# Optimization experiments

Hardware: AMD Instinct MI355X
Metric: run time of the kernel (lower is better)

## Reference

```python
import jax, jax.numpy as jnp
import numpy as np

B, T, D, NH, DK = 2, 2048, 1024, 16, 64
EPS = 1e-6

def proj_H(z):
    return z - z.mean(axis=-1, keepdims=True)

def to_clr(p):
    return proj_H(jnp.log(p + EPS))

def setup_inputs() -> dict:
    key = jax.random.key(0)
    ks = jax.random.split(key, 9)
    p = jax.random.uniform(ks[0], (B, T, D), dtype=jnp.float32)
    # xavier_uniform with gain=0.8 for square-ish [in,out] matrices
    def xavier(k, fan_in, fan_out):
        bound = 0.8 * np.sqrt(6.0 / (fan_in + fan_out))
        return jax.random.uniform(k, (fan_in, fan_out), minval=-bound, maxval=bound, dtype=jnp.float32)
    H = NH * DK
    Wq = xavier(ks[1], D, H); bq = jnp.zeros((H,), jnp.float32)
    Wk = xavier(ks[2], D, H); bk = jnp.zeros((H,), jnp.float32)
    Wv = xavier(ks[3], D, H); bv = jnp.zeros((H,), jnp.float32)
    Wo = xavier(ks[4], H, D); bo = jnp.zeros((D,), jnp.float32)
    return {"p": p, "Wq": Wq, "bq": bq, "Wk": Wk, "bk": bk,
            "Wv": Wv, "bv": bv, "Wo": Wo, "bo": bo}

def reference(p, Wq, bq, Wk, bk, Wv, bv, Wo, bo):
    z = to_clr(p)                                   # [B,T,D]
    # projections with H-projection epilogue, reshaped to [B,T,NH,DK]
    q = proj_H(z @ Wq + bq).reshape(B, T, NH, DK)
    k = proj_H(z @ Wk + bk).reshape(B, T, NH, DK)
    v = proj_H(z @ Wv + bv).reshape(B, T, NH, DK)
    att = jnp.einsum('bihd,bjhd->bhij', q, k) / jnp.sqrt(jnp.float32(DK))
    w = jax.nn.softmax(att, axis=-1)                # dropout is identity in eval
    z_out = jnp.einsum('bhij,bjhd->bihd', w, v).reshape(B, T, NH * DK)
    z_out = proj_H(z_out @ Wo + bo)
    return jax.nn.softmax(z_out, axis=-1)           # from_clr
```

## Files before the change

kernel.cpp:

```cpp
#include <hip/hip_runtime.h>

typedef unsigned short u16;
typedef __attribute__((ext_vector_type(8))) short short8_t;
typedef __attribute__((ext_vector_type(8))) _Float16 half8_t;
typedef __attribute__((ext_vector_type(4))) float f32x4;
typedef __attribute__((ext_vector_type(16))) float f32x16;
typedef __attribute__((ext_vector_type(4))) int int4v;

#define BB    2
#define TT    2048
#define DD    1024
#define NHEAD 16
#define DKH   64
#define HH    1024
#define MR    4096
#define CLR_EPS 1e-6f
#define QSCALE_CONST 0.18033688011112042f

#define O_WQKVT  0ull
#define O_WOT    6291456ull
#define O_WMEAN  8388608ull
#define O_BQKV   8404992ull
#define O_BO     8417280ull
#define O_Z      8421376ull
#define O_QKV    16809984ull
#define O_VT     41975808ull
#define O_ZOUT   50364416ull
#define O_LOGITS O_QKV

__device__ __forceinline__ u16 f2h(float f) {
  _Float16 h = (_Float16)f;
  return __builtin_bit_cast(u16, h);
}
__device__ __forceinline__ float h2f(u16 x) {
  return (float)__builtin_bit_cast(_Float16, x);
}

__device__ __forceinline__ f32x4 mfma16(short8_t a, short8_t b, f32x4 c) {
  return __builtin_amdgcn_mfma_f32_16x16x32_f16(
      __builtin_bit_cast(half8_t, a), __builtin_bit_cast(half8_t, b), c, 0, 0, 0);
}
__device__ __forceinline__ f32x16 mfma32(short8_t a, short8_t b, f32x16 c) {
  return __builtin_amdgcn_mfma_f32_32x32x16_f16(
      __builtin_bit_cast(half8_t, a), __builtin_bit_cast(half8_t, b), c, 0, 0, 0);
}

typedef const __attribute__((address_space(1))) unsigned int as1_u32_t;
typedef __attribute__((address_space(3))) unsigned int as3_u32_t;

__device__ __forceinline__ void async16(const void* g, void* l) {
  __builtin_amdgcn_global_load_lds((as1_u32_t*)g, (as3_u32_t*)l, 16, 0, 0);
}

__device__ __forceinline__ short8_t ldfrag(const u16* buf, int row, int kh, int lane) {
  const int byte = (row * 128 + ((kh * 32 + ((lane >> 4) << 3)) << 1)) ^ ((row & 7) << 4);
  return *(const short8_t*)((const char*)buf + byte);
}

__global__ __launch_bounds__(256) void wprep_mean(
    const float* __restrict__ Wq, const float* __restrict__ Wk,
    const float* __restrict__ Wv, const float* __restrict__ Wo,
    const float* __restrict__ bq, const float* __restrict__ bk,
    const float* __restrict__ bv, const float* __restrict__ bo,
    float* __restrict__ wmean, float* __restrict__ bqkv_p, float* __restrict__ bo_p) {
  __shared__ float sb[4];
  const int bid = blockIdx.x, tid = threadIdx.x;
  if (bid < 4096) {
    const int m = bid >> 10, d = bid & 1023;
    const float* Wm = (m == 0) ? Wq : (m == 1) ? Wk : (m == 2) ? Wv : Wo;
    float4 x = ((const float4*)(Wm + (size_t)d * 1024))[tid];
    float s = x.x + x.y + x.z + x.w;
    #pragma unroll
    for (int dd = 32; dd; dd >>= 1) s += __shfl_xor(s, dd);
    if ((tid & 63) == 0) sb[tid >> 6] = s;
    __syncthreads();
    if (tid == 0) wmean[bid] = (sb[0] + sb[1] + sb[2] + sb[3]) * (1.f / 1024.f);
  } else {
    const int j = bid - 4096;
    const float* bb = (j == 0) ? bq : (j == 1) ? bk : (j == 2) ? bv : bo;
    float4 x = ((const float4*)bb)[tid];
    float s = x.x + x.y + x.z + x.w;
    #pragma unroll
    for (int dd = 32; dd; dd >>= 1) s += __shfl_xor(s, dd);
    if ((tid & 63) == 0) sb[tid >> 6] = s;
    __syncthreads();
    const float mean = (sb[0] + sb[1] + sb[2] + sb[3]) * (1.f / 1024.f);
    float* dst = (j < 3) ? (bqkv_p + j * 1024) : bo_p;
    float4 o = {x.x - mean, x.y - mean, x.z - mean, x.w - mean};
    ((float4*)dst)[tid] = o;
  }
}

__global__ __launch_bounds__(256) void wprep_trans(
    const float* __restrict__ Wq, const float* __restrict__ Wk,
    const float* __restrict__ Wv, const float* __restrict__ Wo,
    const float* __restrict__ wmean, u16* __restrict__ wqkvt, u16* __restrict__ wot) {
  __shared__ float tl[64][65];
  const int tj = blockIdx.x, ti = blockIdx.y, m = blockIdx.z;
  const int tid = threadIdx.x;
  const float* Wm = (m == 0) ? Wq : (m == 1) ? Wk : (m == 2) ? Wv : Wo;
  const int d0 = ti * 64, h0 = tj * 64;
  #pragma unroll
  for (int rr = 0; rr < 4; ++rr) {
    const int r = (tid >> 4) + rr * 16;
    float4 x = *(const float4*)(Wm + (size_t)(d0 + r) * 1024 + h0 + ((tid & 15) << 2));
    const float mu = wmean[m * 1024 + d0 + r];
    tl[r][(tid & 15) * 4 + 0] = x.x - mu;
    tl[r][(tid & 15) * 4 + 1] = x.y - mu;
    tl[r][(tid & 15) * 4 + 2] = x.z - mu;
    tl[r][(tid & 15) * 4 + 3] = x.w - mu;
  }
  __syncthreads();
  #pragma unroll
  for (int rr = 0; rr < 2; ++rr) {
    const int hh = (tid >> 3) + rr * 32;
    const int cd = (tid & 7) << 3;
    short8_t v;
    #pragma unroll
    for (int i = 0; i < 8; ++i) v[i] = (short)f2h(tl[cd + i][hh]);
    u16* dst = (m < 3) ? (wqkvt + ((size_t)(m * 1024 + h0 + hh)) * 1024 + d0 + cd)
                       : (wot + ((size_t)(h0 + hh)) * 1024 + d0 + cd);
    *(short8_t*)dst = v;
  }
}

__global__ __launch_bounds__(256) void clr_kernel(const float* __restrict__ p, u16* __restrict__ z) {
  __shared__ float sb[4];
  const int r = blockIdx.x, tid = threadIdx.x;
  float4 x = ((const float4*)(p + (size_t)r * 1024))[tid];
  float l0 = __logf(x.x + CLR_EPS), l1 = __logf(x.y + CLR_EPS);
  float l2 = __logf(x.z + CLR_EPS), l3 = __logf(x.w + CLR_EPS);
  float s = l0 + l1 + l2 + l3;
  #pragma unroll
  for (int dd = 32; dd; dd >>= 1) s += __shfl_xor(s, dd);
  if ((tid & 63) == 0) sb[tid >> 6] = s;
  __syncthreads();
  const float mu = (sb[0] + sb[1] + sb[2] + sb[3]) * (1.f / 1024.f);
  ushort4 o;
  o.x = f2h(l0 - mu); o.y = f2h(l1 - mu); o.z = f2h(l2 - mu); o.w = f2h(l3 - mu);
  ((ushort4*)(z + (size_t)r * 1024))[tid] = o;
}

__global__ __launch_bounds__(256, 2) void gemm_qkv_8ph(
    const u16* __restrict__ A, const u16* __restrict__ Bt, const float* __restrict__ bias,
    u16* __restrict__ qkv, u16* __restrict__ vt) {
  __shared__ u16 As[2][128 * 64];
  __shared__ u16 Bs[2][192 * 64];
  const int tid = threadIdx.x, lane = tid & 63, w = tid >> 6;
  const int wm = w >> 1, wn = w & 1;
  const int id = blockIdx.x;
  const int x = id & 7, idx = id >> 3;
  const int mt = (x & 3) * 8 + (idx & 7);
  const int nt = (x >> 2) * 8 + (idx >> 3);
  const int m0 = mt * 128, n0 = nt * 192;
  const int srow = tid >> 3, schk = tid & 7;
  const int l15 = lane & 15, lg4 = (lane >> 4) << 2;

  f32x4 acc[4][6] = {};

  auto stA = [&](int k0, int buf) {
    #pragma unroll
    for (int u = 0; u < 4; ++u) {
      const int r = srow + u * 32;
      const int c = k0 + ((schk ^ (r & 7)) << 3);
      async16(A + (size_t)(m0 + r) * 1024 + c, &As[buf][r * 64 + schk * 8]);
    }
  };
  auto stB = [&](int k0, int buf) {
    #pragma unroll
    for (int u = 0; u < 6; ++u) {
      const int r = srow + u * 32;
      const int c = k0 + ((schk ^ (r & 7)) << 3);
      async16(Bt + (size_t)(n0 + r) * 1024 + c, &Bs[buf][r * 64 + schk * 8]);
    }
  };

  stA(0, 0); stB(0, 0);
  asm volatile("s_waitcnt vmcnt(0)" ::: "memory");
  __builtin_amdgcn_s_barrier();

  short8_t afr[4], bfr[6];
  for (int t = 0; t < 16; ++t) {
    const int cur = t & 1;
    const int k0n = ((t + 1) & 15) * 64;
    const u16* Ab = &As[cur][0];
    const u16* Bb_ = &Bs[cur][0];

    #pragma unroll
    for (int j = 0; j < 6; ++j) bfr[j] = ldfrag(Bb_, wn * 96 + j * 16 + l15, 0, lane);
    #pragma unroll
    for (int i = 0; i < 4; ++i) afr[i] = ldfrag(Ab, wm * 64 + i * 16 + l15, 0, lane);
    stA(k0n, cur ^ 1); stB(k0n, cur ^ 1);
    __builtin_amdgcn_s_barrier();
    asm volatile("s_waitcnt lgkmcnt(0)" ::: "memory");
    __builtin_amdgcn_sched_barrier(0);
    __builtin_amdgcn_s_setprio(1);
    #pragma unroll
    for (int i = 0; i < 4; ++i)
      #pragma unroll
      for (int j = 0; j < 6; ++j)
        acc[i][j] = mfma16(afr[i], bfr[j], acc[i][j]);
    __builtin_amdgcn_s_setprio(0);
    __builtin_amdgcn_s_barrier();

    #pragma unroll
    for (int j = 0; j < 6; ++j) bfr[j] = ldfrag(Bb_, wn * 96 + j * 16 + l15, 1, lane);
    #pragma unroll
    for (int i = 0; i < 4; ++i) afr[i] = ldfrag(Ab, wm * 64 + i * 16 + l15, 1, lane);
    __builtin_amdgcn_s_barrier();
    asm volatile("s_waitcnt lgkmcnt(0)" ::: "memory");
    __builtin_amdgcn_sched_barrier(0);
    __builtin_amdgcn_s_setprio(1);
    #pragma unroll
    for (int i = 0; i < 4; ++i)
      #pragma unroll
      for (int j = 0; j < 6; ++j)
        acc[i][j] = mfma16(afr[i], bfr[j], acc[i][j]);
    __builtin_amdgcn_s_setprio(0);
    asm volatile("s_waitcnt vmcnt(0)" ::: "memory");
    __builtin_amdgcn_s_barrier();
  }

  #pragma unroll
  for (int j = 0; j < 6; ++j) {
    const int col = n0 + wn * 96 + j * 16 + l15;
    const float bb = bias[col];
    if (col < 2048) {
      const float sc = (col < 1024) ? QSCALE_CONST : 1.0f;
      #pragma unroll
      for (int i = 0; i < 4; ++i) {
        const int rowb = m0 + wm * 64 + i * 16 + lg4;
        #pragma unroll
        for (int r = 0; r < 4; ++r)
          qkv[(size_t)(rowb + r) * 3072 + col] = f2h((acc[i][j][r] + bb) * sc);
      }
    } else {
      const int h = (col - 2048) >> 6, dk = col & 63;
      #pragma unroll
      for (int i = 0; i < 4; ++i) {
        const int rowb = m0 + wm * 64 + i * 16 + lg4;
        const int b = rowb >> 11, tq = rowb & 2047;
        const int k5 = tq & 31;
        const int pos = (tq & ~31) + (k5 & 16) + ((k5 & 4) << 1) + ((k5 & 8) >> 1);
        ushort4 pk;
        pk.x = f2h(acc[i][j][0] + bb);
        pk.y = f2h(acc[i][j][1] + bb);
        pk.z = f2h(acc[i][j][2] + bb);
        pk.w = f2h(acc[i][j][3] + bb);
        *(ushort4*)(vt + ((size_t)((b * NHEAD + h) * 64 + dk)) * TT + pos) = pk;
      }
    }
  }
}

__global__ __launch_bounds__(256) void gemm_bt(
    const u16* __restrict__ A, const u16* __restrict__ Bt, const float* __restrict__ bias,
    float* __restrict__ Cout, int Ndim, int Kdim) {
  __shared__ u16 As[2][128 * 64];
  __shared__ u16 Bs[2][128 * 64];
  const int tid = threadIdx.x;
  const int lane = tid & 63, wid = tid >> 6;
  const int m0 = blockIdx.y * 128, n0 = blockIdx.x * 128;
  const int wm = wid >> 1, wn = wid & 1;
  const int srow = tid >> 3, schk = tid & 7;
  f32x4 acc[4][4] = {};

  auto STG = [&](int k0, int buf) {
    #pragma unroll
    for (int rr = 0; rr < 4; ++rr) {
      const int row = srow + rr * 32;
      const int gcol = k0 + ((schk ^ (row & 7)) << 3);
      async16(A + (size_t)(m0 + row) * Kdim + gcol, &As[buf][row * 64 + schk * 8]);
      async16(Bt + (size_t)(n0 + row) * Kdim + gcol, &Bs[buf][row * 64 + schk * 8]);
    }
  };

  STG(0, 0);
  asm volatile("s_waitcnt vmcnt(0)" ::: "memory");
  __builtin_amdgcn_s_barrier();

  const int nt = Kdim >> 6;
  for (int t = 0; t < nt; ++t) {
    const int cur = t & 1;
    STG((((t + 1) & (nt - 1))) << 6, cur ^ 1);
    #pragma unroll
    for (int kk = 0; kk < 2; ++kk) {
      short8_t af[4], bf[4];
      #pragma unroll
      for (int i = 0; i < 4; ++i) {
        af[i] = ldfrag(&As[cur][0], wm * 64 + i * 16 + (lane & 15), kk, lane);
        bf[i] = ldfrag(&Bs[cur][0], wn * 64 + i * 16 + (lane & 15), kk, lane);
      }
      #pragma unroll
      for (int i = 0; i < 4; ++i)
        #pragma unroll
        for (int j = 0; j < 4; ++j)
          acc[i][j] = mfma16(af[i], bf[j], acc[i][j]);
    }
    asm volatile("s_waitcnt vmcnt(0)" ::: "memory");
    __builtin_amdgcn_s_barrier();
  }

  #pragma unroll
  for (int j = 0; j < 4; ++j) {
    const int col = n0 + wn * 64 + j * 16 + (lane & 15);
    const float bb = bias[col];
    #pragma unroll
    for (int i = 0; i < 4; ++i) {
      const int rowb = m0 + wm * 64 + i * 16 + ((lane >> 4) << 2);
      #pragma unroll
      for (int r = 0; r < 4; ++r)
        Cout[(size_t)(rowb + r) * Ndim + col] = acc[i][j][r] + bb;
    }
  }
}

__global__ __launch_bounds__(512, 2) void attn_kernel(
    const u16* __restrict__ qkv, const u16* __restrict__ vt, u16* __restrict__ zout) {
  __shared__ char smem[65536];
  const int id = blockIdx.x;
  const int qb = (id >> 3) & 7;
  const int bh = (id & 7) * 4 + (id >> 6);
  const int b = bh >> 4, h = bh & 15;
  const int tid = threadIdx.x, lane = tid & 63, w = tid >> 6;
  const int qw = w & 3, ks = w >> 2;
  const int hl = lane >> 5, l31 = lane & 31;
  const int swz = (l31 & 7) << 4;
  const int q0 = qb * 256 + qw * 64;

  short8_t qf[2][4];
  #pragma unroll
  for (int qt = 0; qt < 2; ++qt)
    #pragma unroll
    for (int c = 0; c < 4; ++c)
      qf[qt][c] = *(const short8_t*)(qkv + (size_t)(b * TT + q0 + qt * 32 + l31) * 3072
                                     + h * 64 + c * 16 + hl * 8);

  const int sr0 = qw * 16 + (lane >> 3);
  const int schk = lane & 7;
  const int scol = (schk ^ (sr0 & 7)) << 3;
  const int dof = sr0 * 128 + schk * 16;
  char* kls = smem + ks * 16384;
  char* vls = smem + 32768 + ks * 16384;
  const u16* kg = qkv + 1024 + (size_t)h * 64;
  const u16* vg = vt + ((size_t)(b * NHEAD + h) * 64 + sr0) * (size_t)TT;

  {
    const int kbase = ks * 1024;
    async16(kg + (size_t)(b * TT + kbase + sr0) * 3072 + scol, kls + dof);
    async16(kg + (size_t)(b * TT + kbase + sr0 + 8) * 3072 + scol, kls + dof + 1024);
    async16(vg + kbase + scol, vls + dof);
    async16(vg + (size_t)8 * TT + kbase + scol, vls + dof + 1024);
  }

  f32x16 o[2][2] = {};
  f32x16 lb[2] = {};
  short8_t ones;
  #pragma unroll
  for (int i = 0; i < 8; ++i) ones[i] = (short)0x3C00;

  for (int it = 0; it < 16; ++it) {
    __syncthreads();
    if (it < 15) {
      const int kbase = ks * 1024 + (it + 1) * 64;
      const int bo = ((it + 1) & 1) * 8192;
      async16(kg + (size_t)(b * TT + kbase + sr0) * 3072 + scol, kls + bo + dof);
      async16(kg + (size_t)(b * TT + kbase + sr0 + 8) * 3072 + scol, kls + bo + dof + 1024);
      async16(vg + kbase + scol, vls + bo + dof);
      async16(vg + (size_t)8 * TT + kbase + scol, vls + bo + dof + 1024);
    }
    const char* Kb = kls + (it & 1) * 8192;
    const char* Vb = vls + (it & 1) * 8192;

    #pragma unroll
    for (int kt = 0; kt < 2; ++kt) {
      f32x16 s[2] = {};
      #pragma unroll
      for (int c = 0; c < 4; ++c) {
        const int krow = kt * 32 + l31;
        const short8_t kfr = *(const short8_t*)(Kb + krow * 128 + ((c * 32 + hl * 16) ^ swz));
        s[0] = mfma32(kfr, qf[0][c], s[0]);
        s[1] = mfma32(kfr, qf[1][c], s[1]);
      }
      #pragma unroll
      for (int qt = 0; qt < 2; ++qt)
        #pragma unroll
        for (int r = 0; r < 16; ++r) {
          float pv;
          asm("v_exp_f32 %0, %1" : "=v"(pv) : "v"(s[qt][r]));
          s[qt][r] = pv;
        }
      #pragma unroll
      for (int cc = 0; cc < 2; ++cc) {
        short8_t pa[2];
        #pragma unroll
        for (int qt = 0; qt < 2; ++qt) {
          int w0 = __builtin_bit_cast(int, __builtin_amdgcn_cvt_pkrtz(s[qt][8 * cc + 0], s[qt][8 * cc + 1]));
          int w1 = __builtin_bit_cast(int, __builtin_amdgcn_cvt_pkrtz(s[qt][8 * cc + 2], s[qt][8 * cc + 3]));
          int w2 = __builtin_bit_cast(int, __builtin_amdgcn_cvt_pkrtz(s[qt][8 * cc + 4], s[qt][8 * cc + 5]));
          int w3 = __builtin_bit_cast(int, __builtin_amdgcn_cvt_pkrtz(s[qt][8 * cc + 6], s[qt][8 * cc + 7]));
          int4v fw = {w0, w1, w2, w3};
          pa[qt] = __builtin_bit_cast(short8_t, fw);
          lb[qt] = mfma32(pa[qt], ones, lb[qt]);
        }
        const int cb = kt * 64 + cc * 32 + hl * 16;
        #pragma unroll
        for (int dkt = 0; dkt < 2; ++dkt) {
          const int vrow = dkt * 32 + l31;
          const short8_t vfr = *(const short8_t*)(Vb + vrow * 128 + (cb ^ swz));
          o[0][dkt] = mfma32(pa[0], vfr, o[0][dkt]);
          o[1][dkt] = mfma32(pa[1], vfr, o[1][dkt]);
        }
      }
    }
  }

  __syncthreads();
  const int slot = qw * 64 + lane;
  if (ks == 1) {
    u16* ro = (u16*)(smem + slot * 136);
    #pragma unroll
    for (int qt = 0; qt < 2; ++qt)
      #pragma unroll
      for (int dkt = 0; dkt < 2; ++dkt)
        #pragma unroll
        for (int r = 0; r < 16; ++r)
          ro[(qt * 2 + dkt) * 16 + r] = f2h(o[qt][dkt][r]);
    u16* rl = (u16*)(smem + 36864 + slot * 72);
    #pragma unroll
    for (int qt = 0; qt < 2; ++qt)
      #pragma unroll
      for (int r = 0; r < 16; ++r)
        rl[qt * 16 + r] = f2h(lb[qt][r]);
  }
  __syncthreads();
  if (ks == 0) {
    const u16* ro = (const u16*)(smem + slot * 136);
    const u16* rl = (const u16*)(smem + 36864 + slot * 72);
    #pragma unroll
    for (int qt = 0; qt < 2; ++qt) {
      #pragma unroll
      for (int r = 0; r < 16; ++r) lb[qt][r] += h2f(rl[qt * 16 + r]);
      #pragma unroll
      for (int dkt = 0; dkt < 2; ++dkt)
        #pragma unroll
        for (int r = 0; r < 16; ++r) o[qt][dkt][r] += h2f(ro[(qt * 2 + dkt) * 16 + r]);
    }
    #pragma unroll
    for (int qt = 0; qt < 2; ++qt) {
      float rlv[16];
      #pragma unroll
      for (int r = 0; r < 16; ++r) rlv[r] = 1.f / lb[qt][r];
      #pragma unroll
      for (int dkt = 0; dkt < 2; ++dkt) {
        const int col = h * 64 + dkt * 32 + l31;
        #pragma unroll
        for (int r = 0; r < 16; ++r) {
          const int rowg = b * TT + q0 + qt * 32 + (r & 3) + 8 * (r >> 2) + 4 * hl;
          zout[(size_t)rowg * 1024 + col] = f2h(o[qt][dkt][r] * rlv[r]);
        }
      }
    }
  }
}

__global__ __launch_bounds__(256) void softmax_rows(const float* __restrict__ logits,
                                                    float* __restrict__ out) {
  __shared__ float sb[8];
  const int r = blockIdx.x, tid = threadIdx.x;
  float4 x = ((const float4*)(logits + (size_t)r * 1024))[tid];
  float mx = fmaxf(fmaxf(x.x, x.y), fmaxf(x.z, x.w));
  #pragma unroll
  for (int dd = 32; dd; dd >>= 1) mx = fmaxf(mx, __shfl_xor(mx, dd));
  if ((tid & 63) == 0) sb[tid >> 6] = mx;
  __syncthreads();
  mx = fmaxf(fmaxf(sb[0], sb[1]), fmaxf(sb[2], sb[3]));
  const float e0 = __expf(x.x - mx), e1 = __expf(x.y - mx);
  const float e2 = __expf(x.z - mx), e3 = __expf(x.w - mx);
  float s = e0 + e1 + e2 + e3;
  #pragma unroll
  for (int dd = 32; dd; dd >>= 1) s += __shfl_xor(s, dd);
  __syncthreads();
  if ((tid & 63) == 0) sb[4 + (tid >> 6)] = s;
  __syncthreads();
  s = sb[4] + sb[5] + sb[6] + sb[7];
  const float inv = 1.f / s;
  float4 o = {e0 * inv, e1 * inv, e2 * inv, e3 * inv};
  ((float4*)(out + (size_t)r * 1024))[tid] = o;
}

extern "C" void kernel_launch(void* const* d_in, const int* in_sizes, int n_in,
                              void* d_out, int out_size, void* d_ws, size_t ws_size,
                              hipStream_t stream) {
  (void)in_sizes; (void)n_in; (void)out_size; (void)ws_size;
  const float* p  = (const float*)d_in[0];
  const float* Wq = (const float*)d_in[1];
  const float* bq = (const float*)d_in[2];
  const float* Wk = (const float*)d_in[3];
  const float* bk = (const float*)d_in[4];
  const float* Wv = (const float*)d_in[5];
  const float* bv = (const float*)d_in[6];
  const float* Wo = (const float*)d_in[7];
  const float* bo = (const float*)d_in[8];
  float* out = (float*)d_out;

  char* ws = (char*)d_ws;
  u16*   wqkvt  = (u16*)(ws + O_WQKVT);
  u16*   wot    = (u16*)(ws + O_WOT);
  float* wmean  = (float*)(ws + O_WMEAN);
  float* bqkv_p = (float*)(ws + O_BQKV);
  float* bo_p   = (float*)(ws + O_BO);
  u16*   z      = (u16*)(ws + O_Z);
  u16*   qkv    = (u16*)(ws + O_QKV);
  u16*   vt     = (u16*)(ws + O_VT);
  u16*   zoutb  = (u16*)(ws + O_ZOUT);
  float* logits = (float*)(ws + O_LOGITS);

  wprep_mean<<<4100, 256, 0, stream>>>(Wq, Wk, Wv, Wo, bq, bk, bv, bo, wmean, bqkv_p, bo_p);
  wprep_trans<<<dim3(16, 16, 4), 256, 0, stream>>>(Wq, Wk, Wv, Wo, wmean, wqkvt, wot);
  clr_kernel<<<MR, 256, 0, stream>>>(p, z);
  gemm_qkv_8ph<<<512, 256, 0, stream>>>(z, wqkvt, bqkv_p, qkv, vt);
  attn_kernel<<<256, 512, 0, stream>>>(qkv, vt, zoutb);
  gemm_bt<<<dim3(1024 / 128, MR / 128), 256, 0, stream>>>(zoutb, wot, bo_p, logits, 1024, 1024);
  softmax_rows<<<MR, 256, 0, stream>>>(logits, out);
}
```

Before: 128.3 us.

## Narrow output GEMM tile to 128x64 and add MFMA priority hints in attention

The output-projection GEMM now uses 128x64 tiles, which doubles the grid from 256 to 512 blocks and adds a launch-bounds occupancy hint of 3 blocks per SM. This targets underfilled CUs on a 256-CU part, at the cost of reloading A tiles twice as often. In the attention kernel, the QK^T MFMAs for both key subtiles are grouped before the exp pass, and s_setprio raises wave priority around the MFMA bursts so matrix work from different waves interleaves with the exp and conversion work. The grouping keeps more score registers live, which can add register pressure.

```diff
diff --git a/kernel.cpp b/kernel.cpp
--- a/kernel.cpp
+++ b/kernel.cpp
@@ -253,17 +253,17 @@
   }
 }
 
-__global__ __launch_bounds__(256) void gemm_bt(
+__global__ __launch_bounds__(256, 3) void gemm_bt(
     const u16* __restrict__ A, const u16* __restrict__ Bt, const float* __restrict__ bias,
     float* __restrict__ Cout, int Ndim, int Kdim) {
   __shared__ u16 As[2][128 * 64];
-  __shared__ u16 Bs[2][128 * 64];
+  __shared__ u16 Bs[2][64 * 64];
   const int tid = threadIdx.x;
   const int lane = tid & 63, wid = tid >> 6;
-  const int m0 = blockIdx.y * 128, n0 = blockIdx.x * 128;
+  const int m0 = blockIdx.y * 128, n0 = blockIdx.x * 64;
   const int wm = wid >> 1, wn = wid & 1;
   const int srow = tid >> 3, schk = tid & 7;
-  f32x4 acc[4][4] = {};
+  f32x4 acc[4][2] = {};
 
   auto STG = [&](int k0, int buf) {
     #pragma unroll
@@ -271,7 +271,8 @@
       const int row = srow + rr * 32;
       const int gcol = k0 + ((schk ^ (row & 7)) << 3);
       async16(A + (size_t)(m0 + row) * Kdim + gcol, &As[buf][row * 64 + schk * 8]);
-      async16(Bt + (size_t)(n0 + row) * Kdim + gcol, &Bs[buf][row * 64 + schk * 8]);
+      if (rr < 2)
+        async16(Bt + (size_t)(n0 + row) * Kdim + gcol, &Bs[buf][row * 64 + schk * 8]);
     }
   };
 
@@ -279,31 +280,34 @@
   asm volatile("s_waitcnt vmcnt(0)" ::: "memory");
   __builtin_amdgcn_s_barrier();
 
-  const int nt = Kdim >> 6;
-  for (int t = 0; t < nt; ++t) {
+  const int ntk = Kdim >> 6;
+  for (int t = 0; t < ntk; ++t) {
     const int cur = t & 1;
-    STG((((t + 1) & (nt - 1))) << 6, cur ^ 1);
+    STG((((t + 1) & (ntk - 1))) << 6, cur ^ 1);
     #pragma unroll
     for (int kk = 0; kk < 2; ++kk) {
-      short8_t af[4], bf[4];
-      #pragma unroll
-      for (int i = 0; i < 4; ++i) {
+      short8_t af[4], bf[2];
+      #pragma unroll
+      for (int i = 0; i < 4; ++i)
         af[i] = ldfrag(&As[cur][0], wm * 64 + i * 16 + (lane & 15), kk, lane);
-        bf[i] = ldfrag(&Bs[cur][0], wn * 64 + i * 16 + (lane & 15), kk, lane);
-      }
+      #pragma unroll
+      for (int j = 0; j < 2; ++j)
+        bf[j] = ldfrag(&Bs[cur][0], wn * 32 + j * 16 + (lane & 15), kk, lane);
+      __builtin_amdgcn_s_setprio(1);
       #pragma unroll
       for (int i = 0; i < 4; ++i)
         #pragma unroll
-        for (int j = 0; j < 4; ++j)
+        for (int j = 0; j < 2; ++j)
           acc[i][j] = mfma16(af[i], bf[j], acc[i][j]);
+      __builtin_amdgcn_s_setprio(0);
     }
     asm volatile("s_waitcnt vmcnt(0)" ::: "memory");
     __builtin_amdgcn_s_barrier();
   }
 
   #pragma unroll
-  for (int j = 0; j < 4; ++j) {
-    const int col = n0 + wn * 64 + j * 16 + (lane & 15);
+  for (int j = 0; j < 2; ++j) {
+    const int col = n0 + wn * 32 + j * 16 + (lane & 15);
     const float bb = bias[col];
     #pragma unroll
     for (int i = 0; i < 4; ++i) {
@@ -372,38 +376,48 @@
     const char* Kb = kls + (it & 1) * 8192;
     const char* Vb = vls + (it & 1) * 8192;
 
+    f32x16 s[2][2] = {};
+    __builtin_amdgcn_s_setprio(1);
     #pragma unroll
     for (int kt = 0; kt < 2; ++kt) {
-      f32x16 s[2] = {};
       #pragma unroll
       for (int c = 0; c < 4; ++c) {
         const int krow = kt * 32 + l31;
         const short8_t kfr = *(const short8_t*)(Kb + krow * 128 + ((c * 32 + hl * 16) ^ swz));
-        s[0] = mfma32(kfr, qf[0][c], s[0]);
-        s[1] = mfma32(kfr, qf[1][c], s[1]);
+        s[kt][0] = mfma32(kfr, qf[0][c], s[kt][0]);
+        s[kt][1] = mfma32(kfr, qf[1][c], s[kt][1]);
       }
+    }
+    __builtin_amdgcn_s_setprio(0);
+
+    #pragma unroll
+    for (int kt = 0; kt < 2; ++kt)
       #pragma unroll
       for (int qt = 0; qt < 2; ++qt)
         #pragma unroll
         for (int r = 0; r < 16; ++r) {
           float pv;
-          asm("v_exp_f32 %0, %1" : "=v"(pv) : "v"(s[qt][r]));
-          s[qt][r] = pv;
+          asm("v_exp_f32 %0, %1" : "=v"(pv) : "v"(s[kt][qt][r]));
+          s[kt][qt][r] = pv;
         }
+
+    #pragma unroll
+    for (int kt = 0; kt < 2; ++kt) {
       #pragma unroll
       for (int cc = 0; cc < 2; ++cc) {
         short8_t pa[2];
         #pragma unroll
         for (int qt = 0; qt < 2; ++qt) {
-          int w0 = __builtin_bit_cast(int, __builtin_amdgcn_cvt_pkrtz(s[qt][8 * cc + 0], s[qt][8 * cc + 1]));
-          int w1 = __builtin_bit_cast(int, __builtin_amdgcn_cvt_pkrtz(s[qt][8 * cc + 2], s[qt][8 * cc + 3]));
-          int w2 = __builtin_bit_cast(int, __builtin_amdgcn_cvt_pkrtz(s[qt][8 * cc + 4], s[qt][8 * cc + 5]));
-          int w3 = __builtin_bit_cast(int, __builtin_amdgcn_cvt_pkrtz(s[qt][8 * cc + 6], s[qt][8 * cc + 7]));
+          int w0 = __builtin_bit_cast(int, __builtin_amdgcn_cvt_pkrtz(s[kt][qt][8 * cc + 0], s[kt][qt][8 * cc + 1]));
+          int w1 = __builtin_bit_cast(int, __builtin_amdgcn_cvt_pkrtz(s[kt][qt][8 * cc + 2], s[kt][qt][8 * cc + 3]));
+          int w2 = __builtin_bit_cast(int, __builtin_amdgcn_cvt_pkrtz(s[kt][qt][8 * cc + 4], s[kt][qt][8 * cc + 5]));
+          int w3 = __builtin_bit_cast(int, __builtin_amdgcn_cvt_pkrtz(s[kt][qt][8 * cc + 6], s[kt][qt][8 * cc + 7]));
           int4v fw = {w0, w1, w2, w3};
           pa[qt] = __builtin_bit_cast(short8_t, fw);
           lb[qt] = mfma32(pa[qt], ones, lb[qt]);
         }
         const int cb = kt * 64 + cc * 32 + hl * 16;
+        __builtin_amdgcn_s_setprio(1);
         #pragma unroll
         for (int dkt = 0; dkt < 2; ++dkt) {
           const int vrow = dkt * 32 + l31;
@@ -411,6 +425,7 @@
           o[0][dkt] = mfma32(pa[0], vfr, o[0][dkt]);
           o[1][dkt] = mfma32(pa[1], vfr, o[1][dkt]);
         }
+        __builtin_amdgcn_s_setprio(0);
       }
     }
   }
@@ -521,6 +536,6 @@
   clr_kernel<<<MR, 256, 0, stream>>>(p, z);
   gemm_qkv_8ph<<<512, 256, 0, stream>>>(z, wqkvt, bqkv_p, qkv, vt);
   attn_kernel<<<256, 512, 0, stream>>>(qkv, vt, zoutb);
-  gemm_bt<<<dim3(1024 / 128, MR / 128), 256, 0, stream>>>(zoutb, wot, bo_p, logits, 1024, 1024);
+  gemm_bt<<<dim3(1024 / 64, MR / 128), 256, 0, stream>>>(zoutb, wot, bo_p, logits, 1024, 1024);
   softmax_rows<<<MR, 256, 0, stream>>>(logits, out);
 }
```

Measured after the change: 119.3 us (median of 2 runs). 1.08x faster.
